# Performance work log

Measured on AMD Instinct MI355X. Metric: run time of the kernel, lower is better.

The kernel has to match this reference:

```python
import jax, jax.numpy as jnp
import numpy as np
from jax import lax

INT32_MAX = 2147483647


def setup_inputs() -> dict:
    key = jax.random.key(0)
    kx, ky = jax.random.split(key)
    x = jax.random.normal(kx, (4096, 64), dtype=jnp.float32)
    y = jax.random.normal(ky, (100000, 64), dtype=jnp.float32)
    return {"x": x, "y": y, "k": 16, "n_splits": 10}


def reference(x, y, k, n_splits):
    """Streaming k-NN: L2 path distance with incremental top-k merge.

    x: (B1, d) queries; y: (B2, d) database. Returns
      ds:  (B1, k)    k smallest distances
      idx: (B1, k, 1) global indices into y (int32), matching (B1,k,y.ndim-1).
    """
    B1, d = x.shape
    B2 = y.shape[0]
    split = B2 // n_splits
    y_splits = y.reshape(n_splits, split, d)  # even splits, as in torch .split
    bases = jnp.arange(n_splits, dtype=jnp.int32) * split

    x2 = jnp.sum(x * x, axis=-1, keepdims=True)  # (B1, 1)

    ds0 = jnp.full((B1, k), jnp.inf, dtype=x.dtype)
    idx0 = jnp.full((B1, k), INT32_MAX, dtype=jnp.int32)
    col = jnp.arange(split, dtype=jnp.int32)

    def step(carry, inp):
        ds, idx = carry
        y_b, base = inp                               # (split, d), scalar
        y2 = jnp.sum(y_b * y_b, axis=-1)              # (split,)
        d2 = x2 + y2[None, :] - 2.0 * (x @ y_b.T)     # (B1, split)
        new_ds = jnp.sqrt(jnp.maximum(d2, 0.0))
        new_idx = jnp.broadcast_to(base + col, (B1, split))
        cat_ds = jnp.concatenate([ds, new_ds], axis=1)      # (B1, k+split)
        cat_idx = jnp.concatenate([idx, new_idx], axis=1)
        neg_top, pos = lax.top_k(-cat_ds, k)                # smallest-k
        ds = -neg_top
        idx = jnp.take_along_axis(cat_idx, pos, axis=1)
        return (ds, idx), None

    (ds, idx), _ = lax.scan(step, (ds0, idx0), (y_splits, bases))
    return ds, idx[..., None]
```

## Files before the change

kernel.cpp:

```cpp
#include <hip/hip_runtime.h>
#include <math.h>

#define D 64
#define K 16
#define NSEG_WANT 128
#define CAP_WANT 512
#define YPAD 128
#define SLOT_B 2304
#define DEPTH 2
#define NGRP 8

typedef __attribute__((ext_vector_type(8))) short short8;
typedef __attribute__((ext_vector_type(4))) float f32x4;

#define SB __builtin_amdgcn_sched_barrier(0)

__device__ __forceinline__ unsigned short f32_to_bf16_rne(float f) {
    unsigned u = __float_as_uint(f);
    u = u + 0x7FFFu + ((u >> 16) & 1u);
    return (unsigned short)(u >> 16);
}

__device__ __forceinline__ void gload16(const void* g, void* l) {
    __builtin_amdgcn_global_load_lds((const __attribute__((address_space(1))) void*)g,
                                     (__attribute__((address_space(3))) void*)l, 16, 0, 0);
}
__device__ __forceinline__ void gload4(const void* g, void* l) {
    __builtin_amdgcn_global_load_lds((const __attribute__((address_space(1))) void*)g,
                                     (__attribute__((address_space(3))) void*)l, 4, 0, 0);
}

__global__ __launch_bounds__(256)
void prep_kernel(const float* __restrict__ x, const float* __restrict__ y,
                 unsigned short* __restrict__ xbneg,
                 unsigned short* __restrict__ yb,
                 float* __restrict__ y2, int B1, int B2)
{
    const int w = threadIdx.x >> 6, lane = threadIdx.x & 63;
    const int row = blockIdx.x * 4 + w;
    const int B2p = B2 + YPAD;
    if (row < B2) {
        const float v = y[(size_t)row * D + lane];
        float s = v * v;
        #pragma unroll
        for (int off = 32; off > 0; off >>= 1) s += __shfl_xor(s, off);
        yb[(size_t)row * D + lane] = f32_to_bf16_rne(v);
        if (lane == 0) y2[row] = s;
    } else if (row < B2p) {
        yb[(size_t)row * D + lane] = 0;
        if (lane == 0) y2[row] = INFINITY;
    } else if (row < B2p + B1) {
        const int r = row - B2p;
        const float v = x[(size_t)r * D + lane];
        xbneg[(size_t)r * D + lane] = f32_to_bf16_rne(-2.0f * v);
    }
}

#define DECODE_BLOCK()                                                       \
    const int id  = blockIdx.x;                                              \
    const int xcd = id & 7;                                                  \
    const int t_  = id >> 3;                                                 \
    const int nqg = B1 >> 8;                                                 \
    const int qi  = t_ % nqg;                                                \
    const int s   = (t_ / nqg) * 8 + xcd;

#define STAGE(slotIdx, c)                                                    \
    do {                                                                     \
        unsigned char* _sb = wl + (slotIdx) * SLOT_B;                        \
        const unsigned short* _g0 = gbase + (size_t)((c) * 16 + 0) * D;      \
        const unsigned short* _g1 = gbase + (size_t)((c) * 16 + 8) * D;      \
        gload16(_g0, _sb);                                                   \
        gload16(_g1, _sb + 1024);                                            \
        gload4(y2g + base + (c) * 16 + lane, _sb + 2048);                    \
    } while (0)

#define WAITSLOT()                                                           \
    do {                                                                     \
        asm volatile("s_waitcnt vmcnt(3)" ::: "memory");                     \
        SB;                                                                  \
    } while (0)

__global__ __launch_bounds__(128, 4)
void knn_min_kernel(const unsigned short* __restrict__ xbneg,
                    const unsigned short* __restrict__ yb,
                    const float* __restrict__ y2g,
                    float* __restrict__ pmin,
                    int B1, int B2, int segsz, int nseg)
{
    const int tid  = threadIdx.x;
    const int w    = tid >> 6;
    const int lane = tid & 63;
    const int n15  = lane & 15;
    const int quad = lane >> 4;
    DECODE_BLOCK();
    const int qb0  = qi * 256 + w * 128;
    const int base = s * segsz;
    const int segN = min(segsz, B2 - base);
    const int nch  = segN >> 4;
    const int nchE = nch & ~1;

    __shared__ __align__(16) unsigned char lds_buf[2 * DEPTH * SLOT_B];
    unsigned char* wl = lds_buf + w * (DEPTH * SLOT_B);

    short8 bA[NGRP], bB[NGRP];
    #pragma unroll
    for (int g = 0; g < NGRP; ++g) {
        const size_t qr = (size_t)(qb0 + g * 16 + n15) * D;
        bA[g] = *(const short8*)&xbneg[qr + quad * 8];
        bB[g] = *(const short8*)&xbneg[qr + 32 + quad * 8];
    }
    SB;

    const int srow  = lane >> 3;
    const int sslot = (lane & 7) ^ srow;
    const unsigned short* gbase = yb + (size_t)(base + srow) * D + (sslot << 3);
    const int roff0 = n15 * 128 + (((quad    ) ^ (n15 & 7)) << 4);
    const int roff1 = n15 * 128 + (((quad + 4) ^ (n15 & 7)) << 4);
    const int yoff  = 2048 + (quad << 4);

    float rm[NGRP];
    #pragma unroll
    for (int g = 0; g < NGRP; ++g) rm[g] = INFINITY;

    STAGE(0, 0); STAGE(1, 1);
    SB;

#define STEP_MIN(slotIdx, c)                                                        \
    do {                                                                            \
        WAITSLOT();                                                                 \
        const unsigned char* _lb = wl + (slotIdx) * SLOT_B;                         \
        const short8 a0 = *(const short8*)(_lb + roff0);                            \
        const short8 a1 = *(const short8*)(_lb + roff1);                            \
        const float4 yv = *(const float4*)(_lb + yoff);                             \
        SB;                                       \
        STAGE(slotIdx, (c) + 2);                    \
        _Pragma("unroll")                                                           \
        for (int g = 0; g < NGRP; ++g) {                                            \
            f32x4 acc = {yv.x, yv.y, yv.z, yv.w};                                   \
            acc = __builtin_amdgcn_mfma_f32_16x16x32_bf16(a0, bA[g], acc, 0, 0, 0); \
            acc = __builtin_amdgcn_mfma_f32_16x16x32_bf16(a1, bB[g], acc, 0, 0, 0); \
            rm[g] = fminf(rm[g], fminf(fminf(acc[0], acc[1]),                       \
                                       fminf(acc[2], acc[3])));                     \
        }                                                                           \
    } while (0)

    for (int ci = 0; ci < nchE; ci += 2) {
        STEP_MIN(0, ci);
        STEP_MIN(1, ci + 1);
    }
    if (nch & 1) STEP_MIN(0, nchE);
#undef STEP_MIN

    asm volatile("s_waitcnt vmcnt(0)" ::: "memory");

    #pragma unroll
    for (int g = 0; g < NGRP; ++g)
        pmin[((size_t)(qb0 + g * 16 + n15) * nseg + s) * 4 + quad] = rm[g];
}

__global__ __launch_bounds__(256)
void knn_thresh_kernel(const float* __restrict__ pmin,
                       float* __restrict__ Tq, int* __restrict__ cnt,
                       int B1, int npart)
{
    const int w    = threadIdx.x >> 6;
    const int lane = threadIdx.x & 63;
    const int q    = blockIdx.x * 4 + w;

    const float* p = pmin + (size_t)q * npart;
    float cd = p[lane];
    float worst = cd;
    #pragma unroll
    for (int off = 32; off > 0; off >>= 1) worst = fmaxf(worst, __shfl_xor(worst, off));

    for (int b = 64; b < npart; b += 64) {
        const float v = p[b + lane];
        for (int j = 0; j < 64; ++j) {
            const float dv = __shfl(v, j);
            if (dv < worst) {
                const unsigned long long m = __ballot(cd == worst);
                const int vict = __ffsll(m) - 1;
                if (lane == vict) cd = dv;
                float wv = cd;
                #pragma unroll
                for (int off = 32; off > 0; off >>= 1) wv = fmaxf(wv, __shfl_xor(wv, off));
                worst = wv;
            }
        }
    }
    if (lane == 0) { Tq[q] = worst; cnt[q] = 0; }
}

__global__ __launch_bounds__(128, 4)
void knn_filter_kernel(const unsigned short* __restrict__ xbneg,
                       const unsigned short* __restrict__ yb,
                       const float* __restrict__ y2g,
                       const float* __restrict__ Tq,
                       int* __restrict__ cnt,
                       float* __restrict__ sd, int* __restrict__ si,
                       int B1, int B2, int segsz, int nseg, int cap)
{
    const int tid  = threadIdx.x;
    const int w    = tid >> 6;
    const int lane = tid & 63;
    const int n15  = lane & 15;
    const int quad = lane >> 4;
    DECODE_BLOCK();
    const int qb0  = qi * 256 + w * 128;
    const int base = s * segsz;
    const int segN = min(segsz, B2 - base);
    const int nch  = segN >> 4;
    const int nchE = nch & ~1;

    __shared__ __align__(16) unsigned char lds_buf[2 * DEPTH * SLOT_B];
    unsigned char* wl = lds_buf + w * (DEPTH * SLOT_B);

    short8 bA[NGRP], bB[NGRP];
    int    qg[NGRP];
    float  th[NGRP];
    #pragma unroll
    for (int g = 0; g < NGRP; ++g) {
        qg[g] = qb0 + g * 16 + n15;
        const size_t qr = (size_t)qg[g] * D;
        bA[g] = *(const short8*)&xbneg[qr + quad * 8];
        bB[g] = *(const short8*)&xbneg[qr + 32 + quad * 8];
        th[g] = Tq[qg[g]];
    }
    SB;

    const int srow  = lane >> 3;
    const int sslot = (lane & 7) ^ srow;
    const unsigned short* gbase = yb + (size_t)(base + srow) * D + (sslot << 3);
    const int roff0 = n15 * 128 + (((quad    ) ^ (n15 & 7)) << 4);
    const int roff1 = n15 * 128 + (((quad + 4) ^ (n15 & 7)) << 4);
    const int yoff  = 2048 + (quad << 4);

    STAGE(0, 0); STAGE(1, 1);
    SB;

#define STEP_FLT(slotIdx, c)                                                        \
    do {                                                                            \
        WAITSLOT();                                                                 \
        const unsigned char* _lb = wl + (slotIdx) * SLOT_B;                         \
        const short8 a0 = *(const short8*)(_lb + roff0);                            \
        const short8 a1 = *(const short8*)(_lb + roff1);                            \
        const float4 yv = *(const float4*)(_lb + yoff);                             \
        SB;                                       \
        STAGE(slotIdx, (c) + 2);                                                    \
        const int cb = base + ((c) << 4) + 4 * quad;                                \
        _Pragma("unroll")                                                           \
        for (int g = 0; g < NGRP; ++g) {                                            \
            f32x4 acc = {yv.x, yv.y, yv.z, yv.w};                                   \
            acc = __builtin_amdgcn_mfma_f32_16x16x32_bf16(a0, bA[g], acc, 0, 0, 0); \
            acc = __builtin_amdgcn_mfma_f32_16x16x32_bf16(a1, bB[g], acc, 0, 0, 0); \
            const float m0 = acc[0];                                                \
            const float m1 = acc[1];                                                \
            const float m2 = acc[2];                                                \
            const float m3 = acc[3];                                                \
            const float mm = fminf(fminf(m0, m1), fminf(m2, m3));                   \
            if (mm <= th[g]) {                                                      \
                const int QQ = qg[g];                                               \
                if (m0 <= th[g]) { const int p_ = atomicAdd(&cnt[QQ], 1); if (p_ < cap) { sd[(size_t)QQ * cap + p_] = m0; si[(size_t)QQ * cap + p_] = cb + 0; } } \
                if (m1 <= th[g]) { const int p_ = atomicAdd(&cnt[QQ], 1); if (p_ < cap) { sd[(size_t)QQ * cap + p_] = m1; si[(size_t)QQ * cap + p_] = cb + 1; } } \
                if (m2 <= th[g]) { const int p_ = atomicAdd(&cnt[QQ], 1); if (p_ < cap) { sd[(size_t)QQ * cap + p_] = m2; si[(size_t)QQ * cap + p_] = cb + 2; } } \
                if (m3 <= th[g]) { const int p_ = atomicAdd(&cnt[QQ], 1); if (p_ < cap) { sd[(size_t)QQ * cap + p_] = m3; si[(size_t)QQ * cap + p_] = cb + 3; } } \
            }                                                                       \
        }                                                                           \
    } while (0)

    for (int ci = 0; ci < nchE; ci += 2) {
        STEP_FLT(0, ci);
        STEP_FLT(1, ci + 1);
    }
    if (nch & 1) STEP_FLT(0, nchE);
#undef STEP_FLT

    asm volatile("s_waitcnt vmcnt(0)" ::: "memory");
}

__global__ __launch_bounds__(256)
void knn_merge_refine_kernel(const float* __restrict__ sd,
                             const int*   __restrict__ si,
                             const int*   __restrict__ cnt,
                             const float* __restrict__ x,
                             const float* __restrict__ y,
                             float* __restrict__ out_ds,
                             float* __restrict__ out_idx,
                             int B1, int B2, int cap)
{
    const int w    = threadIdx.x >> 6;
    const int lane = threadIdx.x & 63;
    const int q    = blockIdx.x * 4 + w;

    float cd = INFINITY;
    int   ci = 2147483647;
    float worst = INFINITY;

    const int n = min(cnt[q], cap);
    const float* sdq = sd + (size_t)q * cap;
    const int*   siq = si + (size_t)q * cap;

    for (int b = 0; b < n; b += 64) {
        const int t = b + lane;
        const float vv = (t < n) ? sdq[t] : INFINITY;
        const int   iv = (t < n) ? siq[t] : 2147483647;
        const int lim = min(64, n - b);
        for (int j = 0; j < lim; ++j) {
            const float dv = __shfl(vv, j);
            if (dv < worst) {
                const int jidx = __shfl(iv, j);
                const unsigned long long m = __ballot(cd == worst);
                const int vict = __ffsll(m) - 1;
                if (lane == vict) { cd = dv; ci = jidx; }
                float wv = cd;
                #pragma unroll
                for (int off = 32; off > 0; off >>= 1)
                    wv = fmaxf(wv, __shfl_xor(wv, off));
                worst = wv;
            }
        }
    }

    __shared__ float xs[4][D];
    __shared__ float sds[4][64];
    __shared__ int   sidx[4][64];

    if (lane < D / 4)
        ((float4*)xs[w])[lane] = ((const float4*)(x + (size_t)q * D))[lane];
    __syncthreads();

    float x2 = 0.f;
    #pragma unroll
    for (int i = 0; i < D; ++i) x2 = __fadd_rn(x2, __fmul_rn(xs[w][i], xs[w][i]));

    int idx = ci;
    float ds32 = INFINITY;
    if (idx >= 0 && idx < B2) {
        float yr[D];
        const float4* yrow = (const float4*)(y + (size_t)idx * D);
        #pragma unroll
        for (int t = 0; t < D / 4; ++t) {
            float4 v = yrow[t];
            yr[4*t+0] = v.x; yr[4*t+1] = v.y; yr[4*t+2] = v.z; yr[4*t+3] = v.w;
        }
        float y2 = 0.f;
        #pragma unroll
        for (int i = 0; i < D; ++i) y2 = __fadd_rn(y2, __fmul_rn(yr[i], yr[i]));

        float dot = 0.f;
        #pragma unroll
        for (int i = 0; i < D; ++i) dot = __fmaf_rn(xs[w][i], yr[i], dot);

        const float d2 = __fsub_rn(__fadd_rn(x2, y2), __fmul_rn(2.0f, dot));
        ds32 = __fsqrt_rn(fmaxf(d2, 0.f));
    } else {
        idx = 2147483647;
    }
    sds[w][lane]  = ds32;
    sidx[w][lane] = idx;
    __syncthreads();

    int rank = 0;
    for (int j = 0; j < 64; ++j) {
        const float dj = sds[w][j];
        bool prec = (dj < ds32);
        if (dj == ds32 && sidx[w][j] != idx) {
            const int  jd    = sidx[w][j];
            const long dd    = (long)jd - (long)idx;
            const long add   = dd < 0 ? -dd : dd;
            const bool t2win = (add >= 21504 && add <= 23552);
            prec = t2win ? (jd > idx) : (jd < idx);
        }
        if (prec) ++rank;
    }
    if (rank < K) {
        out_ds [(size_t)q * K + rank] = ds32;
        out_idx[(size_t)q * K + rank] = (float)idx;
    }
}

extern "C" void kernel_launch(void* const* d_in, const int* in_sizes, int n_in,
                              void* d_out, int out_size, void* d_ws, size_t ws_size,
                              hipStream_t stream)
{
    const float* x = (const float*)d_in[0];
    const float* y = (const float*)d_in[1];

    const int B1 = in_sizes[0] / D;
    const int B2 = in_sizes[1] / D;
    const int B2p = B2 + YPAD;

    const int segsz = (((B2 + NSEG_WANT - 1) / NSEG_WANT) + 15) & ~15;
    const int nseg  = (B2 + segsz - 1) / segsz;

    size_t off = 0;
    unsigned short* xbneg = (unsigned short*)((char*)d_ws + off); off += (size_t)B1 * D * 2;
    unsigned short* yb    = (unsigned short*)((char*)d_ws + off); off += (size_t)B2p * D * 2;
    float*          y2    = (float*)((char*)d_ws + off);          off += (size_t)B2p * 4;
    float*          pmin  = (float*)((char*)d_ws + off);          off += (size_t)B1 * nseg * 4 * 4;
    float*          Tq    = (float*)((char*)d_ws + off);          off += (size_t)B1 * 4;
    int*            cnt   = (int*)((char*)d_ws + off);            off += (size_t)B1 * 4;

    int cap = CAP_WANT;
    {
        const size_t per = (size_t)B1 * 8;
        if (off + (size_t)cap * per > ws_size) {
            const size_t avail = ws_size > off ? ws_size - off : 0;
            cap = (int)(avail / per);
            if (cap < 16) cap = 16;
        }
    }
    float* sd = (float*)((char*)d_ws + off); off += (size_t)B1 * cap * 4;
    int*   si = (int*)((char*)d_ws + off);

    float* out_ds  = (float*)d_out;
    float* out_idx = out_ds + (size_t)B1 * K;

    const int prows = B2p + B1;
    prep_kernel<<<(prows + 3) / 4, 256, 0, stream>>>(x, y, xbneg, yb, y2, B1, B2);

    const int nblk = (B1 / 256) * nseg;
    knn_min_kernel<<<nblk, 128, 0, stream>>>(xbneg, yb, y2, pmin, B1, B2, segsz, nseg);

    knn_thresh_kernel<<<B1 / 4, 256, 0, stream>>>(pmin, Tq, cnt, B1, nseg * 4);

    knn_filter_kernel<<<nblk, 128, 0, stream>>>(xbneg, yb, y2, Tq, cnt, sd, si,
                                                B1, B2, segsz, nseg, cap);

    knn_merge_refine_kernel<<<B1 / 4, 256, 0, stream>>>(sd, si, cnt, x, y,
                                                        out_ds, out_idx,
                                                        B1, B2, cap);
}
```

Baseline: 337.3 us.

## Stage 32 database rows per pipeline step and vectorize the prep kernel

The min and filter kernels now stage 32 y rows per LDS slot instead of 16. Each wait/stage step feeds two independent MFMA chains per query group, which cuts per-chunk wait and issue overhead relative to matrix work. Segment size is rounded to a multiple of 32 with a fixed count of 128 segments. Segments that fall past the end of the database exit early, and the min kernel writes infinity for them. The prep kernel now processes 8 elements per lane with float4 loads and 16-byte bf16 stores. The cost is double the LDS per block and a few idle blocks.

```diff
diff --git a/kernel.cpp b/kernel.cpp
--- a/kernel.cpp
+++ b/kernel.cpp
@@ -3,10 +3,10 @@
 
 #define D 64
 #define K 16
-#define NSEG_WANT 128
+#define NSEG 128
 #define CAP_WANT 512
 #define YPAD 128
-#define SLOT_B 2304
+#define SLOT_B 4352
 #define DEPTH 2
 #define NGRP 8
 
@@ -36,23 +36,41 @@
                  unsigned short* __restrict__ yb,
                  float* __restrict__ y2, int B1, int B2)
 {
-    const int w = threadIdx.x >> 6, lane = threadIdx.x & 63;
-    const int row = blockIdx.x * 4 + w;
-    const int B2p = B2 + YPAD;
+    const int w    = threadIdx.x >> 6;
+    const int lane = threadIdx.x & 63;
+    const int grp  = lane >> 3;
+    const int sub  = lane & 7;
+    const int row  = blockIdx.x * 32 + w * 8 + grp;
+    const int B2p  = B2 + YPAD;
+
     if (row < B2) {
-        const float v = y[(size_t)row * D + lane];
-        float s = v * v;
+        const float4 v0 = *(const float4*)&y[(size_t)row * D + sub * 8];
+        const float4 v1 = *(const float4*)&y[(size_t)row * D + sub * 8 + 4];
+        float s = v0.x*v0.x + v0.y*v0.y + v0.z*v0.z + v0.w*v0.w
+                + v1.x*v1.x + v1.y*v1.y + v1.z*v1.z + v1.w*v1.w;
         #pragma unroll
-        for (int off = 32; off > 0; off >>= 1) s += __shfl_xor(s, off);
-        yb[(size_t)row * D + lane] = f32_to_bf16_rne(v);
-        if (lane == 0) y2[row] = s;
+        for (int off = 4; off > 0; off >>= 1) s += __shfl_xor(s, off);
+        short8 o;
+        o[0] = (short)f32_to_bf16_rne(v0.x); o[1] = (short)f32_to_bf16_rne(v0.y);
+        o[2] = (short)f32_to_bf16_rne(v0.z); o[3] = (short)f32_to_bf16_rne(v0.w);
+        o[4] = (short)f32_to_bf16_rne(v1.x); o[5] = (short)f32_to_bf16_rne(v1.y);
+        o[6] = (short)f32_to_bf16_rne(v1.z); o[7] = (short)f32_to_bf16_rne(v1.w);
+        *(short8*)&yb[(size_t)row * D + sub * 8] = o;
+        if (sub == 0) y2[row] = s;
     } else if (row < B2p) {
-        yb[(size_t)row * D + lane] = 0;
-        if (lane == 0) y2[row] = INFINITY;
+        short8 z = {0,0,0,0,0,0,0,0};
+        *(short8*)&yb[(size_t)row * D + sub * 8] = z;
+        if (sub == 0) y2[row] = INFINITY;
     } else if (row < B2p + B1) {
         const int r = row - B2p;
-        const float v = x[(size_t)r * D + lane];
-        xbneg[(size_t)r * D + lane] = f32_to_bf16_rne(-2.0f * v);
+        const float4 v0 = *(const float4*)&x[(size_t)r * D + sub * 8];
+        const float4 v1 = *(const float4*)&x[(size_t)r * D + sub * 8 + 4];
+        short8 o;
+        o[0] = (short)f32_to_bf16_rne(-2.0f * v0.x); o[1] = (short)f32_to_bf16_rne(-2.0f * v0.y);
+        o[2] = (short)f32_to_bf16_rne(-2.0f * v0.z); o[3] = (short)f32_to_bf16_rne(-2.0f * v0.w);
+        o[4] = (short)f32_to_bf16_rne(-2.0f * v1.x); o[5] = (short)f32_to_bf16_rne(-2.0f * v1.y);
+        o[6] = (short)f32_to_bf16_rne(-2.0f * v1.z); o[7] = (short)f32_to_bf16_rne(-2.0f * v1.w);
+        *(short8*)&xbneg[(size_t)r * D + sub * 8] = o;
     }
 }
 
@@ -67,16 +85,17 @@
 #define STAGE(slotIdx, c)                                                    \
     do {                                                                     \
         unsigned char* _sb = wl + (slotIdx) * SLOT_B;                        \
-        const unsigned short* _g0 = gbase + (size_t)((c) * 16 + 0) * D;      \
-        const unsigned short* _g1 = gbase + (size_t)((c) * 16 + 8) * D;      \
-        gload16(_g0, _sb);                                                   \
-        gload16(_g1, _sb + 1024);                                            \
-        gload4(y2g + base + (c) * 16 + lane, _sb + 2048);                    \
+        const unsigned short* _g = gbase + (size_t)(c) * (32 * D);           \
+        gload16(_g,               _sb);                                      \
+        gload16(_g +  8 * D,      _sb + 1024);                               \
+        gload16(_g + 16 * D,      _sb + 2048);                               \
+        gload16(_g + 24 * D,      _sb + 3072);                               \
+        gload4(y2g + base + (c) * 32 + lane, _sb + 4096);                    \
     } while (0)
 
 #define WAITSLOT()                                                           \
     do {                                                                     \
-        asm volatile("s_waitcnt vmcnt(3)" ::: "memory");                     \
+        asm volatile("s_waitcnt vmcnt(5)" ::: "memory");                     \
         SB;                                                                  \
     } while (0)
 
@@ -96,8 +115,15 @@
     const int qb0  = qi * 256 + w * 128;
     const int base = s * segsz;
     const int segN = min(segsz, B2 - base);
-    const int nch  = segN >> 4;
+    const int nch  = (segN > 0) ? (segN >> 5) : 0;
     const int nchE = nch & ~1;
+
+    if (nch <= 0) {
+        #pragma unroll
+        for (int g = 0; g < NGRP; ++g)
+            pmin[((size_t)(qb0 + g * 16 + n15) * nseg + s) * 4 + quad] = INFINITY;
+        return;
+    }
 
     __shared__ __align__(16) unsigned char lds_buf[2 * DEPTH * SLOT_B];
     unsigned char* wl = lds_buf + w * (DEPTH * SLOT_B);
@@ -116,7 +142,7 @@
     const unsigned short* gbase = yb + (size_t)(base + srow) * D + (sslot << 3);
     const int roff0 = n15 * 128 + (((quad    ) ^ (n15 & 7)) << 4);
     const int roff1 = n15 * 128 + (((quad + 4) ^ (n15 & 7)) << 4);
-    const int yoff  = 2048 + (quad << 4);
+    const int yoff  = 4096 + (quad << 4);
 
     float rm[NGRP];
     #pragma unroll
@@ -131,16 +157,24 @@
         const unsigned char* _lb = wl + (slotIdx) * SLOT_B;                         \
         const short8 a0 = *(const short8*)(_lb + roff0);                            \
         const short8 a1 = *(const short8*)(_lb + roff1);                            \
-        const float4 yv = *(const float4*)(_lb + yoff);                             \
+        const short8 a2 = *(const short8*)(_lb + 2048 + roff0);                     \
+        const short8 a3 = *(const short8*)(_lb + 2048 + roff1);                     \
+        const float4 yv1 = *(const float4*)(_lb + yoff);                            \
+        const float4 yv2 = *(const float4*)(_lb + 64 + yoff);                       \
         SB;                                       \
         STAGE(slotIdx, (c) + 2);                    \
         _Pragma("unroll")                                                           \
         for (int g = 0; g < NGRP; ++g) {                                            \
-            f32x4 acc = {yv.x, yv.y, yv.z, yv.w};                                   \
+            f32x4 acc = {yv1.x, yv1.y, yv1.z, yv1.w};                               \
             acc = __builtin_amdgcn_mfma_f32_16x16x32_bf16(a0, bA[g], acc, 0, 0, 0); \
             acc = __builtin_amdgcn_mfma_f32_16x16x32_bf16(a1, bB[g], acc, 0, 0, 0); \
+            f32x4 acd = {yv2.x, yv2.y, yv2.z, yv2.w};                               \
+            acd = __builtin_amdgcn_mfma_f32_16x16x32_bf16(a2, bA[g], acd, 0, 0, 0); \
+            acd = __builtin_amdgcn_mfma_f32_16x16x32_bf16(a3, bB[g], acd, 0, 0, 0); \
             rm[g] = fminf(rm[g], fminf(fminf(acc[0], acc[1]),                       \
                                        fminf(acc[2], acc[3])));                     \
+            rm[g] = fminf(rm[g], fminf(fminf(acd[0], acd[1]),                       \
+                                       fminf(acd[2], acd[3])));                     \
         }                                                                           \
     } while (0)
 
@@ -209,8 +243,10 @@
     const int qb0  = qi * 256 + w * 128;
     const int base = s * segsz;
     const int segN = min(segsz, B2 - base);
-    const int nch  = segN >> 4;
+    const int nch  = (segN > 0) ? (segN >> 5) : 0;
     const int nchE = nch & ~1;
+
+    if (nch <= 0) return;
 
     __shared__ __align__(16) unsigned char lds_buf[2 * DEPTH * SLOT_B];
     unsigned char* wl = lds_buf + w * (DEPTH * SLOT_B);
@@ -233,10 +269,21 @@
     const unsigned short* gbase = yb + (size_t)(base + srow) * D + (sslot << 3);
     const int roff0 = n15 * 128 + (((quad    ) ^ (n15 & 7)) << 4);
     const int roff1 = n15 * 128 + (((quad + 4) ^ (n15 & 7)) << 4);
-    const int yoff  = 2048 + (quad << 4);
+    const int yoff  = 4096 + (quad << 4);
 
     STAGE(0, 0); STAGE(1, 1);
     SB;
+
+#define APPEND4(M0, M1, M2, M3, TH, QQ, CB)                                         \
+    do {                                                                            \
+        const float mm_ = fminf(fminf(M0, M1), fminf(M2, M3));                      \
+        if (mm_ <= (TH)) {                                                          \
+            if (M0 <= (TH)) { const int p_ = atomicAdd(&cnt[QQ], 1); if (p_ < cap) { sd[(size_t)(QQ) * cap + p_] = M0; si[(size_t)(QQ) * cap + p_] = (CB) + 0; } } \
+            if (M1 <= (TH)) { const int p_ = atomicAdd(&cnt[QQ], 1); if (p_ < cap) { sd[(size_t)(QQ) * cap + p_] = M1; si[(size_t)(QQ) * cap + p_] = (CB) + 1; } } \
+            if (M2 <= (TH)) { const int p_ = atomicAdd(&cnt[QQ], 1); if (p_ < cap) { sd[(size_t)(QQ) * cap + p_] = M2; si[(size_t)(QQ) * cap + p_] = (CB) + 2; } } \
+            if (M3 <= (TH)) { const int p_ = atomicAdd(&cnt[QQ], 1); if (p_ < cap) { sd[(size_t)(QQ) * cap + p_] = M3; si[(size_t)(QQ) * cap + p_] = (CB) + 3; } } \
+        }                                                                           \
+    } while (0)
 
 #define STEP_FLT(slotIdx, c)                                                        \
     do {                                                                            \
@@ -244,27 +291,24 @@
         const unsigned char* _lb = wl + (slotIdx) * SLOT_B;                         \
         const short8 a0 = *(const short8*)(_lb + roff0);                            \
         const short8 a1 = *(const short8*)(_lb + roff1);                            \
-        const float4 yv = *(const float4*)(_lb + yoff);                             \
+        const short8 a2 = *(const short8*)(_lb + 2048 + roff0);                     \
+        const short8 a3 = *(const short8*)(_lb + 2048 + roff1);                     \
+        const float4 yv1 = *(const float4*)(_lb + yoff);                            \
+        const float4 yv2 = *(const float4*)(_lb + 64 + yoff);                       \
         SB;                                       \
         STAGE(slotIdx, (c) + 2);                                                    \
-        const int cb = base + ((c) << 4) + 4 * quad;                                \
+        const int cb1 = base + ((c) << 5) + 4 * quad;                               \
+        const int cb2 = cb1 + 16;                                                   \
         _Pragma("unroll")                                                           \
         for (int g = 0; g < NGRP; ++g) {                                            \
-            f32x4 acc = {yv.x, yv.y, yv.z, yv.w};                                   \
+            f32x4 acc = {yv1.x, yv1.y, yv1.z, yv1.w};                               \
             acc = __builtin_amdgcn_mfma_f32_16x16x32_bf16(a0, bA[g], acc, 0, 0, 0); \
             acc = __builtin_amdgcn_mfma_f32_16x16x32_bf16(a1, bB[g], acc, 0, 0, 0); \
-            const float m0 = acc[0];                                                \
-            const float m1 = acc[1];                                                \
-            const float m2 = acc[2];                                                \
-            const float m3 = acc[3];                                                \
-            const float mm = fminf(fminf(m0, m1), fminf(m2, m3));                   \
-            if (mm <= th[g]) {                                                      \
-                const int QQ = qg[g];                                               \
-                if (m0 <= th[g]) { const int p_ = atomicAdd(&cnt[QQ], 1); if (p_ < cap) { sd[(size_t)QQ * cap + p_] = m0; si[(size_t)QQ * cap + p_] = cb + 0; } } \
-                if (m1 <= th[g]) { const int p_ = atomicAdd(&cnt[QQ], 1); if (p_ < cap) { sd[(size_t)QQ * cap + p_] = m1; si[(size_t)QQ * cap + p_] = cb + 1; } } \
-                if (m2 <= th[g]) { const int p_ = atomicAdd(&cnt[QQ], 1); if (p_ < cap) { sd[(size_t)QQ * cap + p_] = m2; si[(size_t)QQ * cap + p_] = cb + 2; } } \
-                if (m3 <= th[g]) { const int p_ = atomicAdd(&cnt[QQ], 1); if (p_ < cap) { sd[(size_t)QQ * cap + p_] = m3; si[(size_t)QQ * cap + p_] = cb + 3; } } \
-            }                                                                       \
+            f32x4 acd = {yv2.x, yv2.y, yv2.z, yv2.w};                               \
+            acd = __builtin_amdgcn_mfma_f32_16x16x32_bf16(a2, bA[g], acd, 0, 0, 0); \
+            acd = __builtin_amdgcn_mfma_f32_16x16x32_bf16(a3, bB[g], acd, 0, 0, 0); \
+            APPEND4(acc[0], acc[1], acc[2], acc[3], th[g], qg[g], cb1);             \
+            APPEND4(acd[0], acd[1], acd[2], acd[3], th[g], qg[g], cb2);             \
         }                                                                           \
     } while (0)
 
@@ -274,6 +318,7 @@
     }
     if (nch & 1) STEP_FLT(0, nchE);
 #undef STEP_FLT
+#undef APPEND4
 
     asm volatile("s_waitcnt vmcnt(0)" ::: "memory");
 }
@@ -390,8 +435,8 @@
     const int B2 = in_sizes[1] / D;
     const int B2p = B2 + YPAD;
 
-    const int segsz = (((B2 + NSEG_WANT - 1) / NSEG_WANT) + 15) & ~15;
-    const int nseg  = (B2 + segsz - 1) / segsz;
+    const int segsz = (((B2 + NSEG - 1) / NSEG) + 31) & ~31;
+    const int nseg  = NSEG;
 
     size_t off = 0;
     unsigned short* xbneg = (unsigned short*)((char*)d_ws + off); off += (size_t)B1 * D * 2;
@@ -417,7 +462,7 @@
     float* out_idx = out_ds + (size_t)B1 * K;
 
     const int prows = B2p + B1;
-    prep_kernel<<<(prows + 3) / 4, 256, 0, stream>>>(x, y, xbneg, yb, y2, B1, B2);
+    prep_kernel<<<(prows + 31) / 32, 256, 0, stream>>>(x, y, xbneg, yb, y2, B1, B2);
 
     const int nblk = (B1 / 256) * nseg;
     knn_min_kernel<<<nblk, 128, 0, stream>>>(xbneg, yb, y2, pmin, B1, B2, segsz, nseg);
```

Measured after the change: 386.3 us. 1.15x slower.
